# Kernel optimization log

Measured on AMD Instinct MI355X. Metric: run time of the kernel, lower is better.

Reference implementation:

```python
import jax, jax.numpy as jnp
import numpy as np

N_NODES = 100000
N_EDGES = 1600000
IN_DIM, HID_DIM, OUT_DIM = 128, 128, 64


def setup_inputs() -> dict:
    key = jax.random.key(0)
    ks = jax.random.split(key, 8)
    x = jax.random.normal(ks[0], (N_NODES, IN_DIM), dtype=jnp.float32)
    edge_index = jax.random.randint(ks[1], (2, N_EDGES), 0, N_NODES, dtype=jnp.int64)
    sc = 0.05
    W1 = jax.random.normal(ks[2], (IN_DIM, HID_DIM), dtype=jnp.float32) * sc
    b1 = jnp.zeros((HID_DIM,), dtype=jnp.float32)
    W2 = jax.random.normal(ks[3], (HID_DIM, HID_DIM), dtype=jnp.float32) * sc
    b2 = jnp.zeros((HID_DIM,), dtype=jnp.float32)
    W3 = jax.random.normal(ks[4], (HID_DIM, OUT_DIM), dtype=jnp.float32) * sc
    b3 = jnp.zeros((OUT_DIM,), dtype=jnp.float32)
    return {"x": x, "edge_index": edge_index, "W1": W1, "b1": b1,
            "W2": W2, "b2": b2, "W3": W3, "b3": b3}


def _gcn_conv(x, src, dst, norm, W, b, n_nodes):
    # x' = D^{-1/2} (A + I) D^{-1/2} (x W) + b   (PyG GCNConv default)
    h = x @ W                                   # [N, F_out]
    msg = h[src] * norm[:, None]                # gather + scale, [E+N, F_out]
    agg = jax.ops.segment_sum(msg, dst, num_segments=n_nodes)  # scatter-add
    return agg + b


def _build_norm(edge_index, n_nodes):
    # add self-loops, compute symmetric normalization coefficients
    loops = jnp.arange(n_nodes, dtype=edge_index.dtype)
    src = jnp.concatenate([edge_index[0], loops])
    dst = jnp.concatenate([edge_index[1], loops])
    deg = jax.ops.segment_sum(jnp.ones_like(dst, dtype=jnp.float32), dst,
                              num_segments=n_nodes)
    dinv = jnp.where(deg > 0, jax.lax.rsqrt(jnp.maximum(deg, 1.0)), 0.0)
    norm = dinv[src] * dinv[dst]
    return src, dst, norm


def reference(x, edge_index, W1, b1, W2, b2, W3, b3):
    n = x.shape[0]
    src, dst, norm = _build_norm(edge_index, n)
    h = jax.nn.relu(_gcn_conv(x, src, dst, norm, W1, b1, n))
    h = jax.nn.relu(_gcn_conv(h, src, dst, norm, W2, b2, n))
    out = _gcn_conv(h, src, dst, norm, W3, b3, n)
    return out
```

## Files before the change

kernel.cpp:

```cpp
#include <hip/hip_runtime.h>
#include <hip/hip_fp16.h>
#include <cstdint>
#include <cstddef>
#include <type_traits>

#define NN 100000
#define NE 1600000
#define SCAN_BLOCKS ((NN + 1023) / 1024)
#define NBK ((NN + 255) / 256)
#define BCAP 4608
#define EPB 4096
#define BIN_BLOCKS ((NE + EPB - 1) / EPB)

using half8 = __attribute__((ext_vector_type(8))) _Float16;
using f32x4 = __attribute__((ext_vector_type(4))) float;

union F4H8 { float4 f4; __half2 h2[4]; };

__device__ __forceinline__ uint2 pack4half(float4 v) {
    __half2 a = __floats2half2_rn(v.x, v.y);
    __half2 b = __floats2half2_rn(v.z, v.w);
    uint2 r;
    r.x = *(unsigned int*)&a;
    r.y = *(unsigned int*)&b;
    return r;
}

__device__ __forceinline__ void acc8(float* acc, const F4H8& u) {
#pragma unroll
    for (int k = 0; k < 4; k++) {
        float2 f = __half22float2(u.h2[k]);
        acc[2 * k] += f.x;
        acc[2 * k + 1] += f.y;
    }
}

__global__ void detect_flag_kernel(const int* __restrict__ idx, int* __restrict__ flag) {
    __shared__ int cnt;
    if (threadIdx.x == 0) cnt = 0;
    __syncthreads();
    if (idx[2 * threadIdx.x + 1] == 0) atomicAdd(&cnt, 1);
    __syncthreads();
    if (threadIdx.x == 0) *flag = (cnt == (int)blockDim.x) ? 1 : 0;
}

__global__ __launch_bounds__(256) void bin_kernel(const void* __restrict__ idx,
                                                  const int* __restrict__ flag,
                                                  int* __restrict__ gcnt,
                                                  int* __restrict__ bucketbuf) {
    __shared__ int cnt[NBK];
    __shared__ int gbase[NBK];
    int t = threadIdx.x;
    long long base = (long long)blockIdx.x * EPB;
    for (int i = t; i < NBK; i += 256) cnt[i] = 0;
    __syncthreads();
    bool is64 = (*flag != 0);
    int lpos[16], d16[16], s16[16];
#pragma unroll
    for (int j = 0; j < 16; j++) {
        long long e = base + j * 256 + t;
        lpos[j] = 0; d16[j] = 0; s16[j] = 0;
        if (e < NE) {
            int s_, d_;
            if (is64) { const long long* p = (const long long*)idx; s_ = (int)p[e]; d_ = (int)p[NE + e]; }
            else      { const int* p = (const int*)idx;             s_ = p[e];      d_ = p[NE + e]; }
            d16[j] = d_; s16[j] = s_;
            lpos[j] = atomicAdd(&cnt[d_ >> 8], 1);
        }
    }
    __syncthreads();
    for (int b = t; b < NBK; b += 256) {
        int c = cnt[b];
        gbase[b] = (c > 0) ? atomicAdd(&gcnt[b * 16], c) : 0;
    }
    __syncthreads();
#pragma unroll
    for (int j = 0; j < 16; j++) {
        long long e = base + j * 256 + t;
        if (e < NE) {
            int b = d16[j] >> 8;
            int pos = gbase[b] + lpos[j];
            if (pos < BCAP) bucketbuf[(size_t)b * BCAP + pos] = (s16[j] << 8) | (d16[j] & 255);
        }
    }
}

__global__ __launch_bounds__(256) void hist_kernel(const int* __restrict__ gcnt,
                                                   const int* __restrict__ bucketbuf,
                                                   int* __restrict__ deg,
                                                   float* __restrict__ dinv) {
    __shared__ int cnt[256];
    int t = threadIdx.x, b = blockIdx.x;
    cnt[t] = 0;
    __syncthreads();
    int n = gcnt[b * 16]; if (n > BCAP) n = BCAP;
    for (int i = t; i < n; i += 256)
        atomicAdd(&cnt[bucketbuf[(size_t)b * BCAP + i] & 255], 1);
    __syncthreads();
    int node = b * 256 + t;
    if (node < NN) {
        int d = cnt[t];
        deg[node] = d;
        dinv[node] = rsqrtf((float)(d + 1));
    }
}

__global__ __launch_bounds__(256) void scanA_kernel(const int* __restrict__ deg,
                                                    int* __restrict__ blocksum) {
    __shared__ int red[256];
    int t = threadIdx.x;
    int base = blockIdx.x * 1024 + t * 4;
    int s = 0;
#pragma unroll
    for (int j = 0; j < 4; j++) { int i = base + j; if (i < NN) s += deg[i]; }
    red[t] = s;
    __syncthreads();
    for (int off = 128; off > 0; off >>= 1) {
        if (t < off) red[t] += red[t + off];
        __syncthreads();
    }
    if (t == 0) blocksum[blockIdx.x] = red[0];
}

__global__ __launch_bounds__(256) void scanC_kernel(const int* __restrict__ deg,
                                                    const int* __restrict__ blocksum,
                                                    int* __restrict__ row_start) {
    __shared__ int lds[256];
    __shared__ int boff_s;
    int t = threadIdx.x;
    int b = blockIdx.x;
    lds[t] = (t < b && t < SCAN_BLOCKS) ? blocksum[t] : 0;
    __syncthreads();
    for (int off = 128; off > 0; off >>= 1) {
        if (t < off) lds[t] += lds[t + off];
        __syncthreads();
    }
    if (t == 0) boff_s = lds[0];
    __syncthreads();
    int boff = boff_s;

    int base = b * 1024 + t * 4;
    int d[4]; int s = 0;
#pragma unroll
    for (int j = 0; j < 4; j++) { int i = base + j; d[j] = (i < NN) ? deg[i] : 0; s += d[j]; }
    __syncthreads();
    lds[t] = s;
    __syncthreads();
    for (int off = 1; off < 256; off <<= 1) {
        int u = (t >= off) ? lds[t - off] : 0;
        __syncthreads();
        lds[t] += u;
        __syncthreads();
    }
    int offr = boff + ((t == 0) ? 0 : lds[t - 1]);
#pragma unroll
    for (int j = 0; j < 4; j++) {
        int i = base + j;
        if (i < NN) { row_start[i] = offr; offr += d[j]; }
    }
    if (b == 0 && t == 0) row_start[NN] = NE;
}

__global__ __launch_bounds__(256) void csrfill_kernel(const int* __restrict__ gcnt,
                                                      const int* __restrict__ bucketbuf,
                                                      const int* __restrict__ row_start,
                                                      int* __restrict__ csr) {
    __shared__ int cur[256];
    int t = threadIdx.x, b = blockIdx.x;
    int node = b * 256 + t;
    cur[t] = (node < NN) ? row_start[node] : 0;
    __syncthreads();
    int n = gcnt[b * 16]; if (n > BCAP) n = BCAP;
    for (int i = t; i < n; i += 256) {
        int v = bucketbuf[(size_t)b * BCAP + i];
        int pos = atomicAdd(&cur[v & 255], 1);
        csr[pos] = v >> 8;
    }
}

__global__ __launch_bounds__(256) void dhist_kernel(const int* __restrict__ deg,
                                                    int* __restrict__ dbins) {
    __shared__ int h[256];
    int t = threadIdx.x;
    h[t] = 0;
    __syncthreads();
    int i = blockIdx.x * 256 + t;
    if (i < NN) {
        int d = deg[i]; if (d > 255) d = 255;
        atomicAdd(&h[d], 1);
    }
    __syncthreads();
    if (h[t] > 0) atomicAdd(&dbins[t], h[t]);
}

__global__ void dscan_kernel(const int* __restrict__ dbins, int* __restrict__ dstart) {
    __shared__ int lds[256];
    int t = threadIdx.x;
    lds[t] = dbins[t];
    __syncthreads();
    if (t == 0) {
        int s = 0;
        for (int i = 0; i < 256; i++) { int v = lds[i]; lds[i] = s; s += v; }
    }
    __syncthreads();
    dstart[t] = lds[t];
}

__global__ __launch_bounds__(256) void dscatter_kernel(const int* __restrict__ deg,
                                                       int* __restrict__ dstart,
                                                       int* __restrict__ perm) {
    __shared__ int h[256];
    __shared__ int base[256];
    int t = threadIdx.x;
    h[t] = 0;
    __syncthreads();
    int i = blockIdx.x * 256 + t;
    int d = 0, lpos = 0;
    bool valid = (i < NN);
    if (valid) {
        d = deg[i]; if (d > 255) d = 255;
        lpos = atomicAdd(&h[d], 1);
    }
    __syncthreads();
    base[t] = (h[t] > 0) ? atomicAdd(&dstart[t], h[t]) : 0;
    __syncthreads();
    if (valid) perm[base[d] + lpos] = i;
}

__global__ void wt_kernel(const float* __restrict__ W, __half* __restrict__ Wt, int F) {
    int i = blockIdx.x * 256 + threadIdx.x;
    if (i >= 128 * F) return;
    int k = i / F, n = i % F;
    Wt[(size_t)n * 128 + k] = __float2half(W[i]);
}

template <int F, typename AT>
__global__ __launch_bounds__(256) void mfma_gemm_kernel(const AT* __restrict__ A,
                                                        const __half* __restrict__ Wt,
                                                        const float* __restrict__ dinv,
                                                        __half* __restrict__ H, int N) {
    constexpr int K = 128;
    constexpr int NT = F / 16;
    constexpr int FP = F + 8;
    __shared__ __half hs[64 * FP];

    int wave = threadIdx.x >> 6;
    int lane = threadIdx.x & 63;
    int quad = lane >> 4;
    int l16  = lane & 15;
    int rowbase = blockIdx.x * 64 + wave * 16;
    int arow = rowbase + l16; if (arow >= N) arow = N - 1;

    half8 afrag[4];
    const AT* ap = A + (size_t)arow * K + quad * 8;
#pragma unroll
    for (int s = 0; s < 4; s++) {
        if constexpr (std::is_same<AT, float>::value) {
            float4 u0 = *(const float4*)(ap + s * 32);
            float4 u1 = *(const float4*)(ap + s * 32 + 4);
            half8 h;
            h[0] = (_Float16)u0.x; h[1] = (_Float16)u0.y;
            h[2] = (_Float16)u0.z; h[3] = (_Float16)u0.w;
            h[4] = (_Float16)u1.x; h[5] = (_Float16)u1.y;
            h[6] = (_Float16)u1.z; h[7] = (_Float16)u1.w;
            afrag[s] = h;
        } else {
            afrag[s] = *(const half8*)(ap + s * 32);
        }
    }

    f32x4 acc[NT];
#pragma unroll
    for (int t = 0; t < NT; t++) acc[t] = (f32x4){0.f, 0.f, 0.f, 0.f};

#pragma unroll
    for (int s = 0; s < 4; s++) {
#pragma unroll
        for (int t = 0; t < NT; t++) {
            half8 b = *(const half8*)(Wt + (size_t)(t * 16 + l16) * K + s * 32 + quad * 8);
            acc[t] = __builtin_amdgcn_mfma_f32_16x16x32_f16(afrag[s], b, acc[t], 0, 0, 0);
        }
    }

    float dv[4];
#pragma unroll
    for (int r = 0; r < 4; r++) {
        int grow = rowbase + quad * 4 + r;
        dv[r] = (grow < N) ? dinv[grow] : 0.f;
    }
#pragma unroll
    for (int t = 0; t < NT; t++) {
#pragma unroll
        for (int r = 0; r < 4; r++) {
            int lrow = wave * 16 + quad * 4 + r;
            hs[lrow * FP + t * 16 + l16] = __float2half(acc[t][r] * dv[r]);
        }
    }
    __syncthreads();
    constexpr int CHUNKS = 64 * F / 8;
    for (int i = threadIdx.x; i < CHUNKS; i += 256) {
        int row = i / (F / 8);
        int col8 = (i % (F / 8)) * 8;
        int grow = blockIdx.x * 64 + row;
        if (grow < N)
            *(uint4*)&H[(size_t)grow * F + col8] = *(const uint4*)&hs[row * FP + col8];
    }
}

template <int FO>
__global__ __launch_bounds__(256) void agg_gemm_kernel(const __half* __restrict__ Hs,
                                                       const int* __restrict__ rs,
                                                       const int* __restrict__ csr,
                                                       const float* __restrict__ dinv,
                                                       const float* __restrict__ bias,
                                                       const __half* __restrict__ Wt,
                                                       const int* __restrict__ perm,
                                                       __half* __restrict__ Hout) {
    constexpr int FI = 128;
    constexpr int FP = FI + 8;
    constexpr int FPO = FO + 8;
    constexpr int NT4 = FO / 64;
    __shared__ __half Alds[16 * FP];
    __shared__ int nids[16];

    int tid = threadIdx.x;
    int nodebase = blockIdx.x * 16;
    if (tid < 16) nids[tid] = perm[nodebase + tid];
    __syncthreads();
    int lrow = tid / 16;
    int node = nids[lrow];
    int q = (tid % 16) * 8;

    float dn = dinv[node];
    float acc[8];
    {
        F4H8 u; u.f4 = *(const float4*)&Hs[(size_t)node * FI + q];
#pragma unroll
        for (int j = 0; j < 4; j++) {
            float2 f = __half22float2(u.h2[j]);
            acc[2 * j] = f.x; acc[2 * j + 1] = f.y;
        }
    }
    int e = rs[node];
    int e1 = rs[node + 1];
    for (; e + 8 <= e1; e += 8) {
        int s[8];
#pragma unroll
        for (int j = 0; j < 8; j++) s[j] = csr[e + j];
        F4H8 h[8];
#pragma unroll
        for (int j = 0; j < 8; j++) h[j].f4 = *(const float4*)&Hs[(size_t)s[j] * FI + q];
#pragma unroll
        for (int j = 0; j < 8; j++) acc8(acc, h[j]);
    }
    for (; e < e1; e++) {
        int s = csr[e];
        F4H8 u; u.f4 = *(const float4*)&Hs[(size_t)s * FI + q];
        acc8(acc, u);
    }
    float4 b0 = *(const float4*)&bias[q];
    float4 b1 = *(const float4*)&bias[q + 4];
    float o[8];
    o[0] = fmaxf(dn * acc[0] + b0.x, 0.f); o[1] = fmaxf(dn * acc[1] + b0.y, 0.f);
    o[2] = fmaxf(dn * acc[2] + b0.z, 0.f); o[3] = fmaxf(dn * acc[3] + b0.w, 0.f);
    o[4] = fmaxf(dn * acc[4] + b1.x, 0.f); o[5] = fmaxf(dn * acc[5] + b1.y, 0.f);
    o[6] = fmaxf(dn * acc[6] + b1.z, 0.f); o[7] = fmaxf(dn * acc[7] + b1.w, 0.f);
    {
        uint4 p;
        uint2 a = pack4half(make_float4(o[0], o[1], o[2], o[3]));
        uint2 b = pack4half(make_float4(o[4], o[5], o[6], o[7]));
        p.x = a.x; p.y = a.y; p.z = b.x; p.w = b.y;
        *(uint4*)&Alds[lrow * FP + q] = p;
    }
    __syncthreads();

    int wave = tid >> 6;
    int lane = tid & 63;
    int quad = lane >> 4;
    int l16  = lane & 15;

    half8 afrag[4];
#pragma unroll
    for (int s = 0; s < 4; s++)
        afrag[s] = *(const half8*)&Alds[l16 * FP + s * 32 + quad * 8];

    f32x4 cacc[NT4];
#pragma unroll
    for (int t = 0; t < NT4; t++) cacc[t] = (f32x4){0.f, 0.f, 0.f, 0.f};
#pragma unroll
    for (int s = 0; s < 4; s++) {
#pragma unroll
        for (int t = 0; t < NT4; t++) {
            int tile = wave * NT4 + t;
            half8 b = *(const half8*)(Wt + (size_t)(tile * 16 + l16) * FI + s * 32 + quad * 8);
            cacc[t] = __builtin_amdgcn_mfma_f32_16x16x32_f16(afrag[s], b, cacc[t], 0, 0, 0);
        }
    }
    __syncthreads();

    float dv[4];
#pragma unroll
    for (int r = 0; r < 4; r++) dv[r] = dinv[nids[quad * 4 + r]];
#pragma unroll
    for (int t = 0; t < NT4; t++) {
        int colb = (wave * NT4 + t) * 16 + l16;
#pragma unroll
        for (int r = 0; r < 4; r++)
            Alds[(quad * 4 + r) * FPO + colb] = __float2half(cacc[t][r] * dv[r]);
    }
    __syncthreads();
    constexpr int CHUNKS = 16 * FO / 8;
    for (int i = tid; i < CHUNKS; i += 256) {
        int row = i / (FO / 8);
        int col8 = (i % (FO / 8)) * 8;
        *(uint4*)&Hout[(size_t)nids[row] * FO + col8] = *(const uint4*)&Alds[row * FPO + col8];
    }
}

template <int F>
__global__ __launch_bounds__(256) void agg_kernel(const __half* __restrict__ Hs,
                                                  const int* __restrict__ rs,
                                                  const int* __restrict__ csr,
                                                  const float* __restrict__ dinv,
                                                  const float* __restrict__ bias,
                                                  const int* __restrict__ perm,
                                                  float* __restrict__ OUT) {
    constexpr int CQ = F / 8;
    constexpr int NPB = 256 / CQ;
    int pidx = blockIdx.x * NPB + threadIdx.x / CQ;
    if (pidx >= NN) return;
    int node = perm[pidx];
    int q = (threadIdx.x % CQ) * 8;
    float dn = dinv[node];
    float acc[8];
    {
        F4H8 u; u.f4 = *(const float4*)&Hs[(size_t)node * F + q];
#pragma unroll
        for (int j = 0; j < 4; j++) {
            float2 f = __half22float2(u.h2[j]);
            acc[2 * j] = f.x; acc[2 * j + 1] = f.y;
        }
    }
    int e = rs[node];
    int e1 = rs[node + 1];
    for (; e + 8 <= e1; e += 8) {
        int s[8];
#pragma unroll
        for (int j = 0; j < 8; j++) s[j] = csr[e + j];
        F4H8 h[8];
#pragma unroll
        for (int j = 0; j < 8; j++) h[j].f4 = *(const float4*)&Hs[(size_t)s[j] * F + q];
#pragma unroll
        for (int j = 0; j < 8; j++) acc8(acc, h[j]);
    }
    for (; e < e1; e++) {
        int s = csr[e];
        F4H8 u; u.f4 = *(const float4*)&Hs[(size_t)s * F + q];
        acc8(acc, u);
    }
    float4 o0 = make_float4(dn * acc[0] + bias[q],     dn * acc[1] + bias[q + 1],
                            dn * acc[2] + bias[q + 2], dn * acc[3] + bias[q + 3]);
    float4 o1 = make_float4(dn * acc[4] + bias[q + 4], dn * acc[5] + bias[q + 5],
                            dn * acc[6] + bias[q + 6], dn * acc[7] + bias[q + 7]);
    *(float4*)&OUT[(size_t)node * F + q]     = o0;
    *(float4*)&OUT[(size_t)node * F + q + 4] = o1;
}

extern "C" void kernel_launch(void* const* d_in, const int* in_sizes, int n_in,
                              void* d_out, int out_size, void* d_ws, size_t ws_size,
                              hipStream_t stream) {
    const float* x  = (const float*)d_in[0];
    const void* eidx = d_in[1];
    const float* W1 = (const float*)d_in[2];
    const float* b1 = (const float*)d_in[3];
    const float* W2 = (const float*)d_in[4];
    const float* b2 = (const float*)d_in[5];
    const float* W3 = (const float*)d_in[6];
    const float* b3 = (const float*)d_in[7];
    float* out = (float*)d_out;

    char* ws = (char*)d_ws;
    size_t off = 0;
    auto alloc = [&](size_t bytes) -> void* {
        void* p = ws + off;
        off += (bytes + 255) & ~(size_t)255;
        return p;
    };
    __half* bufA = (__half*)alloc((size_t)NN * 128 * 2);
    int* bucketbuf = (int*)bufA;
    int* gcnt      = (int*)((char*)bufA + (size_t)NBK * BCAP * 4);
    __half* bufC = (__half*)alloc((size_t)NN * 128 * 2);
    int* deg      = (int*)bufC;
    int* blocksum = (int*)((char*)bufC + (size_t)NN * 4);
    int* row_start = (int*)alloc((size_t)(NN + 1) * 4);
    float* dinv = (float*)alloc((size_t)NN * 4);
    int* flagp  = (int*)alloc(256);
    int* csr    = (int*)alloc((size_t)NE * 4);
    int* perm   = (int*)alloc((size_t)NN * 4);
    int* dbins  = (int*)alloc(256 * 4);
    int* dstart = (int*)alloc(256 * 4);
    __half* Wt1 = (__half*)alloc((size_t)128 * 128 * 2);
    __half* Wt2 = (__half*)alloc((size_t)128 * 128 * 2);
    __half* Wt3 = (__half*)alloc((size_t)64 * 128 * 2);

    hipMemsetAsync(gcnt, 0, (size_t)NBK * 16 * 4, stream);
    hipMemsetAsync(dbins, 0, 256 * 4, stream);
    detect_flag_kernel<<<1, 256, 0, stream>>>((const int*)eidx, flagp);
    bin_kernel<<<BIN_BLOCKS, 256, 0, stream>>>(eidx, flagp, gcnt, bucketbuf);
    hist_kernel<<<NBK, 256, 0, stream>>>(gcnt, bucketbuf, deg, dinv);
    scanA_kernel<<<SCAN_BLOCKS, 256, 0, stream>>>(deg, blocksum);
    scanC_kernel<<<SCAN_BLOCKS, 256, 0, stream>>>(deg, blocksum, row_start);
    csrfill_kernel<<<NBK, 256, 0, stream>>>(gcnt, bucketbuf, row_start, csr);

    dhist_kernel<<<NBK, 256, 0, stream>>>(deg, dbins);
    dscan_kernel<<<1, 256, 0, stream>>>(dbins, dstart);
    dscatter_kernel<<<NBK, 256, 0, stream>>>(deg, dstart, perm);

    wt_kernel<<<(128 * 128 + 255) / 256, 256, 0, stream>>>(W1, Wt1, 128);
    wt_kernel<<<(128 * 128 + 255) / 256, 256, 0, stream>>>(W2, Wt2, 128);
    wt_kernel<<<(128 * 64 + 255) / 256, 256, 0, stream>>>(W3, Wt3, 64);

    const int GB = (NN + 63) / 64;
    mfma_gemm_kernel<128, float><<<GB, 256, 0, stream>>>(x, Wt1, dinv, bufA, NN);
    agg_gemm_kernel<128><<<NN / 16, 256, 0, stream>>>(bufA, row_start, csr, dinv, b1, Wt2, perm, bufC);
    agg_gemm_kernel<64><<<NN / 16, 256, 0, stream>>>(bufC, row_start, csr, dinv, b2, Wt3, perm, bufA);
    agg_kernel<64><<<NN / 32, 256, 0, stream>>>(bufA, row_start, csr, dinv, b3, perm, out);
}
```

Before: 380.1 us.

## Reorder CSR rows into degree-permuted order and sort neighbor lists

Builds a second CSR whose rows follow the degree-sorted permutation (new prefix scan over perm) and sorts each row's source indices with insertion sort. The aggregation kernels then read row offsets and neighbor indices contiguously per block and gather in ascending source order, aiming for better index-load coalescing and cache locality on feature gathers. It adds three preprocessing kernels, an extra NE-sized buffer, and a serial per-thread sort whose cost grows with row length.

```diff
diff --git a/kernel.cpp b/kernel.cpp
--- a/kernel.cpp
+++ b/kernel.cpp
@@ -225,6 +225,84 @@
     base[t] = (h[t] > 0) ? atomicAdd(&dstart[t], h[t]) : 0;
     __syncthreads();
     if (valid) perm[base[d] + lpos] = i;
+}
+
+__global__ __launch_bounds__(256) void scanAp_kernel(const int* __restrict__ deg,
+                                                     const int* __restrict__ perm,
+                                                     int* __restrict__ blocksum) {
+    __shared__ int red[256];
+    int t = threadIdx.x;
+    int base = blockIdx.x * 1024 + t * 4;
+    int s = 0;
+#pragma unroll
+    for (int j = 0; j < 4; j++) { int i = base + j; if (i < NN) s += deg[perm[i]]; }
+    red[t] = s;
+    __syncthreads();
+    for (int off = 128; off > 0; off >>= 1) {
+        if (t < off) red[t] += red[t + off];
+        __syncthreads();
+    }
+    if (t == 0) blocksum[blockIdx.x] = red[0];
+}
+
+__global__ __launch_bounds__(256) void scanCp_kernel(const int* __restrict__ deg,
+                                                     const int* __restrict__ perm,
+                                                     const int* __restrict__ blocksum,
+                                                     int* __restrict__ prs) {
+    __shared__ int lds[256];
+    __shared__ int boff_s;
+    int t = threadIdx.x;
+    int b = blockIdx.x;
+    lds[t] = (t < b && t < SCAN_BLOCKS) ? blocksum[t] : 0;
+    __syncthreads();
+    for (int off = 128; off > 0; off >>= 1) {
+        if (t < off) lds[t] += lds[t + off];
+        __syncthreads();
+    }
+    if (t == 0) boff_s = lds[0];
+    __syncthreads();
+    int boff = boff_s;
+
+    int base = b * 1024 + t * 4;
+    int d[4]; int s = 0;
+#pragma unroll
+    for (int j = 0; j < 4; j++) { int i = base + j; d[j] = (i < NN) ? deg[perm[i]] : 0; s += d[j]; }
+    __syncthreads();
+    lds[t] = s;
+    __syncthreads();
+    for (int off = 1; off < 256; off <<= 1) {
+        int u = (t >= off) ? lds[t - off] : 0;
+        __syncthreads();
+        lds[t] += u;
+        __syncthreads();
+    }
+    int offr = boff + ((t == 0) ? 0 : lds[t - 1]);
+#pragma unroll
+    for (int j = 0; j < 4; j++) {
+        int i = base + j;
+        if (i < NN) { prs[i] = offr; offr += d[j]; }
+    }
+    if (b == 0 && t == 0) prs[NN] = NE;
+}
+
+__global__ __launch_bounds__(256) void rowsort_kernel(const int* __restrict__ rs,
+                                                      const int* __restrict__ csr,
+                                                      const int* __restrict__ perm,
+                                                      const int* __restrict__ prs,
+                                                      int* __restrict__ pcsr) {
+    int pidx = blockIdx.x * 256 + threadIdx.x;
+    if (pidx >= NN) return;
+    int node = perm[pidx];
+    int e = rs[node];
+    int n = rs[node + 1] - e;
+    int o = prs[pidx];
+    for (int j = 0; j < n; j++) pcsr[o + j] = csr[e + j];
+    for (int j = 1; j < n; j++) {
+        int v = pcsr[o + j];
+        int k = j - 1;
+        while (k >= 0 && pcsr[o + k] > v) { pcsr[o + k + 1] = pcsr[o + k]; k--; }
+        pcsr[o + k + 1] = v;
+    }
 }
 
 __global__ void wt_kernel(const float* __restrict__ W, __half* __restrict__ Wt, int F) {
@@ -309,8 +387,8 @@
 
 template <int FO>
 __global__ __launch_bounds__(256) void agg_gemm_kernel(const __half* __restrict__ Hs,
-                                                       const int* __restrict__ rs,
-                                                       const int* __restrict__ csr,
+                                                       const int* __restrict__ prs,
+                                                       const int* __restrict__ pcsr,
                                                        const float* __restrict__ dinv,
                                                        const float* __restrict__ bias,
                                                        const __half* __restrict__ Wt,
@@ -341,12 +419,12 @@
             acc[2 * j] = f.x; acc[2 * j + 1] = f.y;
         }
     }
-    int e = rs[node];
-    int e1 = rs[node + 1];
+    int e = prs[nodebase + lrow];
+    int e1 = prs[nodebase + lrow + 1];
     for (; e + 8 <= e1; e += 8) {
         int s[8];
 #pragma unroll
-        for (int j = 0; j < 8; j++) s[j] = csr[e + j];
+        for (int j = 0; j < 8; j++) s[j] = pcsr[e + j];
         F4H8 h[8];
 #pragma unroll
         for (int j = 0; j < 8; j++) h[j].f4 = *(const float4*)&Hs[(size_t)s[j] * FI + q];
@@ -354,7 +432,7 @@
         for (int j = 0; j < 8; j++) acc8(acc, h[j]);
     }
     for (; e < e1; e++) {
-        int s = csr[e];
+        int s = pcsr[e];
         F4H8 u; u.f4 = *(const float4*)&Hs[(size_t)s * FI + q];
         acc8(acc, u);
     }
@@ -419,8 +497,8 @@
 
 template <int F>
 __global__ __launch_bounds__(256) void agg_kernel(const __half* __restrict__ Hs,
-                                                  const int* __restrict__ rs,
-                                                  const int* __restrict__ csr,
+                                                  const int* __restrict__ prs,
+                                                  const int* __restrict__ pcsr,
                                                   const float* __restrict__ dinv,
                                                   const float* __restrict__ bias,
                                                   const int* __restrict__ perm,
@@ -441,12 +519,12 @@
             acc[2 * j] = f.x; acc[2 * j + 1] = f.y;
         }
     }
-    int e = rs[node];
-    int e1 = rs[node + 1];
+    int e = prs[pidx];
+    int e1 = prs[pidx + 1];
     for (; e + 8 <= e1; e += 8) {
         int s[8];
 #pragma unroll
-        for (int j = 0; j < 8; j++) s[j] = csr[e + j];
+        for (int j = 0; j < 8; j++) s[j] = pcsr[e + j];
         F4H8 h[8];
 #pragma unroll
         for (int j = 0; j < 8; j++) h[j].f4 = *(const float4*)&Hs[(size_t)s[j] * F + q];
@@ -454,7 +532,7 @@
         for (int j = 0; j < 8; j++) acc8(acc, h[j]);
     }
     for (; e < e1; e++) {
-        int s = csr[e];
+        int s = pcsr[e];
         F4H8 u; u.f4 = *(const float4*)&Hs[(size_t)s * F + q];
         acc8(acc, u);
     }
@@ -499,6 +577,8 @@
     int* perm   = (int*)alloc((size_t)NN * 4);
     int* dbins  = (int*)alloc(256 * 4);
     int* dstart = (int*)alloc(256 * 4);
+    int* prs    = (int*)alloc((size_t)(NN + 1) * 4);
+    int* pcsr   = (int*)alloc((size_t)NE * 4);
     __half* Wt1 = (__half*)alloc((size_t)128 * 128 * 2);
     __half* Wt2 = (__half*)alloc((size_t)128 * 128 * 2);
     __half* Wt3 = (__half*)alloc((size_t)64 * 128 * 2);
@@ -515,6 +595,9 @@
     dhist_kernel<<<NBK, 256, 0, stream>>>(deg, dbins);
     dscan_kernel<<<1, 256, 0, stream>>>(dbins, dstart);
     dscatter_kernel<<<NBK, 256, 0, stream>>>(deg, dstart, perm);
+    scanAp_kernel<<<SCAN_BLOCKS, 256, 0, stream>>>(deg, perm, blocksum);
+    scanCp_kernel<<<SCAN_BLOCKS, 256, 0, stream>>>(deg, perm, blocksum, prs);
+    rowsort_kernel<<<NBK, 256, 0, stream>>>(row_start, csr, perm, prs, pcsr);
 
     wt_kernel<<<(128 * 128 + 255) / 256, 256, 0, stream>>>(W1, Wt1, 128);
     wt_kernel<<<(128 * 128 + 255) / 256, 256, 0, stream>>>(W2, Wt2, 128);
@@ -522,7 +605,7 @@
 
     const int GB = (NN + 63) / 64;
     mfma_gemm_kernel<128, float><<<GB, 256, 0, stream>>>(x, Wt1, dinv, bufA, NN);
-    agg_gemm_kernel<128><<<NN / 16, 256, 0, stream>>>(bufA, row_start, csr, dinv, b1, Wt2, perm, bufC);
-    agg_gemm_kernel<64><<<NN / 16, 256, 0, stream>>>(bufC, row_start, csr, dinv, b2, Wt3, perm, bufA);
-    agg_kernel<64><<<NN / 32, 256, 0, stream>>>(bufA, row_start, csr, dinv, b3, perm, out);
-}
+    agg_gemm_kernel<128><<<NN / 16, 256, 0, stream>>>(bufA, prs, pcsr, dinv, b1, Wt2, perm, bufC);
+    agg_gemm_kernel<64><<<NN / 16, 256, 0, stream>>>(bufC, prs, pcsr, dinv, b2, Wt3, perm, bufA);
+    agg_kernel<64><<<NN / 32, 256, 0, stream>>>(bufA, prs, pcsr, dinv, b3, perm, out);
+}
```

Measured after the change: 521.1 us. 37.1% more time.
